# Optimization experiments

Hardware: AMD Instinct MI355X
Metric: run time of the kernel (lower is better)

The kernel has to match this reference:

```python
import jax, jax.numpy as jnp
import numpy as np

DIM = 1024
SCALE = DIM ** (-0.5)
TEMPERATURE = 1.0


def setup_inputs() -> dict:
    key = jax.random.key(0)
    ks = jax.random.split(key, 7)
    B, N, D = 8, 4096, DIM
    s = 1.0 / np.sqrt(D)
    return {
        "x": jax.random.normal(ks[0], (B, N, D), dtype=jnp.float32),
        "Wq": jax.random.normal(ks[1], (D, D), dtype=jnp.float32) * s,
        "bq": jax.random.normal(ks[2], (D,), dtype=jnp.float32) * 0.01,
        "Wk": jax.random.normal(ks[3], (D, D), dtype=jnp.float32) * s,
        "bk": jax.random.normal(ks[4], (D,), dtype=jnp.float32) * 0.01,
        "Wv": jax.random.normal(ks[5], (D, D), dtype=jnp.float32) * s,
        "bv": jax.random.normal(ks[6], (D,), dtype=jnp.float32) * 0.01,
    }


def reference(x, Wq, bq, Wk, bk, Wv, bv):
    B, N, D = x.shape
    # adaptive_avg_pool1d from N -> N//2 with N even == mean over adjacent pairs
    q_input = x.reshape(B, N // 2, 2, D).mean(axis=2)  # [B, N/2, D]
    # torch Linear: y = x @ W.T + b
    q = jnp.einsum("bmd,ed->bme", q_input, Wq) + bq      # [B, N/2, D]
    k = jnp.einsum("bnd,ed->bne", x, Wk) + bk            # [B, N, D]
    v = jnp.einsum("bnd,ed->bne", x, Wv) + bv            # [B, N, D]
    attn = jnp.einsum("bmd,bnd->bmn", q, k) * SCALE      # [B, N/2, N]
    attn = jax.nn.softmax(attn * TEMPERATURE, axis=-1)
    k_out = jnp.einsum("bmn,bnd->bmd", attn, v)          # [B, N/2, D]
    return (q, k_out, k_out)
```

## Files before the change

### kernel.cpp

```cpp
#include <hip/hip_runtime.h>
#include <hip/hip_bf16.h>
#include <cstddef>

typedef __attribute__((ext_vector_type(8))) short s16x8;
typedef __attribute__((ext_vector_type(4))) short s16x4;
typedef __attribute__((ext_vector_type(4))) float f32x4;

#define MFMA_BF16(a, b, c) __builtin_amdgcn_mfma_f32_16x16x32_bf16((a), (b), (c), 0, 0, 0)

__device__ __forceinline__ short f2bf(float f) {
    union { float f; unsigned u; } cv; cv.f = f;
    unsigned u = cv.u;
    unsigned r = (u + 0x7FFFu + ((u >> 16) & 1u)) >> 16;
    return (short)r;
}
__device__ __forceinline__ float bf2f(unsigned short u) {
    union { unsigned u; float f; } cv; cv.u = ((unsigned)u) << 16; return cv.f;
}

__device__ __forceinline__ void gl16(const void* g, void* l) {
    __builtin_amdgcn_global_load_lds(
        (const __attribute__((address_space(1))) void*)g,
        (__attribute__((address_space(3))) void*)l, 16, 0, 0);
}

template <int MODE>
__global__ __launch_bounds__(256, 2) void gemm_bf(
    const void* __restrict__ Ap, const short* __restrict__ Bp,
    const float* __restrict__ bias, const float* __restrict__ lvec,
    void* __restrict__ Cp, void* __restrict__ Cp2,
    int zbase, float* __restrict__ lpart)
{
    constexpr int NT  = (MODE == 4 || MODE == 7) ? 64 : 16;
    constexpr int LDA = (MODE == 4 || MODE == 7) ? 4096 : 1024;
    constexpr int LDB = (MODE == 4 || MODE == 7) ? 4096 : 1024;

    __shared__ short As[128 * 64];
    __shared__ short Bs[128 * 64];
    const int tid = threadIdx.x;

    int bx, by, z;
    if constexpr (MODE == 6) {
        const int swz = (blockIdx.x & 7) * 256 + (blockIdx.x >> 3);
        by = swz % 16; bx = (swz / 16) % 32; z = swz / 512 + zbase;
    } else if constexpr (MODE == 7) {
        const int swz = (blockIdx.x & 7) * 64 + (blockIdx.x >> 3);
        by = swz % 16; bx = (swz / 16) % 8; z = swz / 128 + zbase;
    } else if constexpr (MODE == 0) {
        const int swz = (blockIdx.x & 7) * 256 + (blockIdx.x >> 3);
        bx = swz & 7; by = swz >> 3; z = 0;
    } else if constexpr (MODE == 1) {
        const int swz = (blockIdx.x & 7) * 256 + (blockIdx.x >> 3);
        by = swz % 8; bx = (swz / 8) % 32; z = swz / 256;
    } else if constexpr (MODE == 3 || MODE == 4 || MODE == 5) {
        const int n = blockIdx.x;
        z = n & 7; const int m = n >> 3; by = m % 16; bx = m / 16;
    } else { bx = blockIdx.x; by = blockIdx.y; z = blockIdx.z; }

    const int w = tid >> 6, l = tid & 63, l15 = l & 15, lhi = l >> 4;
    const int wy = w >> 1, wx = w & 1;
    const int X = (l15 & 7) << 3;
    const int lr8 = l >> 3, cb = l & 7, scb = cb ^ lr8;

    size_t arow0 = (size_t)by * 128, brow0 = (size_t)bx * 128;
    if constexpr (MODE == 3 || MODE == 4 || MODE == 5 || MODE == 6) arow0 += (size_t)z * 2048;
    if constexpr (MODE == 7) arow0 += (size_t)(z & 3) * 2048;
    if constexpr (MODE == 1 || MODE == 3 || MODE == 5 || MODE == 6) brow0 += (size_t)z * 4096;
    if constexpr (MODE == 4 || MODE == 7) brow0 += (size_t)z * 1024;

    const short* Ab = (const short*)Ap;
    const float* Af = (const float*)Ap;

    const short* gA = Ab + (arow0 + w * 32 + lr8) * (size_t)LDA + scb * 8;
    const short* gB = Bp + (brow0 + w * 32 + lr8) * (size_t)LDB + scb * 8;

    f32x4 acc[4][4];
    #pragma unroll
    for (int m = 0; m < 4; ++m)
        #pragma unroll
        for (int n = 0; n < 4; ++n) acc[m][n] = (f32x4){0.f, 0.f, 0.f, 0.f};

    const int r0b = tid >> 3, cb8 = (tid & 7) * 8;
    const int r0f = tid >> 4, kcs = tid & 15;

    for (int kt = 0; kt < NT; ++kt) {
        #pragma unroll
        for (int i = 0; i < 4; ++i)
            gl16(gB + (size_t)(i * 8) * LDB + kt * 64, &Bs[(w * 32 + i * 8) * 64]);
        if constexpr (MODE == 2) {
            #pragma unroll
            for (int p = 0; p < 4; ++p) {
                const int r = r0b + p * 32;
                const size_t g = (arow0 + r) * 2048 + kt * 64 + cb8;
                s16x8 u0 = *(const s16x8*)(Ab + g);
                s16x8 u1 = *(const s16x8*)(Ab + g + 1024);
                s16x8 o;
                #pragma unroll
                for (int j = 0; j < 8; ++j)
                    o[j] = f2bf(0.5f * (bf2f((unsigned short)u0[j]) + bf2f((unsigned short)u1[j])));
                *(s16x8*)&As[r * 64 + (cb8 ^ ((r & 7) * 8))] = o;
            }
        } else if constexpr (MODE == 3) {
            const int k0 = kt * 64 + kcs * 4;
            #pragma unroll
            for (int p = 0; p < 8; ++p) {
                const int r = r0f + p * 16;
                float4 u = *(const float4*)(Af + (arow0 + r) * 1024 + k0);
                s16x4 sa = { f2bf(u.x * 0.03125f), f2bf(u.y * 0.03125f),
                             f2bf(u.z * 0.03125f), f2bf(u.w * 0.03125f) };
                *(s16x4*)&As[r * 64 + ((kcs * 4) ^ ((r & 7) * 8))] = sa;
            }
        } else {
            #pragma unroll
            for (int i = 0; i < 4; ++i)
                gl16(gA + (size_t)(i * 8) * LDA + kt * 64, &As[(w * 32 + i * 8) * 64]);
        }
        __syncthreads();
        #pragma unroll
        for (int kk = 0; kk < 2; ++kk) {
            const int e = (kk * 32 + lhi * 8) ^ X;
            s16x8 af[4], bfr[4];
            #pragma unroll
            for (int m = 0; m < 4; ++m)
                af[m] = *(const s16x8*)&As[(wy * 64 + m * 16 + l15) * 64 + e];
            #pragma unroll
            for (int n = 0; n < 4; ++n)
                bfr[n] = *(const s16x8*)&Bs[(wx * 64 + n * 16 + l15) * 64 + e];
            #pragma unroll
            for (int m = 0; m < 4; ++m)
                #pragma unroll
                for (int n = 0; n < 4; ++n)
                    acc[m][n] = MFMA_BF16(af[m], bfr[n], acc[m][n]);
        }
        __syncthreads();
    }

    #pragma unroll
    for (int m = 0; m < 4; ++m) {
        #pragma unroll
        for (int j = 0; j < 4; ++j) {
            const int rl = wy * 64 + m * 16 + lhi * 4 + j;
            const int grow = by * 128 + rl;
            float radd = 0.f, rmul = 1.f;
            if constexpr (MODE == 1) radd = bias[grow];
            if constexpr (MODE == 4 || MODE == 7) rmul = 1.0f / lvec[(size_t)z * 2048 + grow];
            if constexpr (MODE == 6) {
                float s = 0.f;
                #pragma unroll
                for (int n = 0; n < 4; ++n) {
                    const int gcol = bx * 128 + wx * 64 + n * 16 + l15;
                    const float pv = __expf(acc[m][n][j]);
                    s += pv;
                    ((short*)Cp)[(size_t)(z & 3) * 8388608 + (size_t)grow * 4096 + gcol] = f2bf(pv);
                }
                s += __shfl_xor(s, 1);
                s += __shfl_xor(s, 2);
                s += __shfl_xor(s, 4);
                s += __shfl_xor(s, 8);
                if (l15 == 0)
                    lpart[((size_t)(z & 3) * 2048 + grow) * 64 + bx * 2 + wx] = s;
            } else {
                #pragma unroll
                for (int n = 0; n < 4; ++n) {
                    const int cl = wx * 64 + n * 16 + l15;
                    const int gcol = bx * 128 + cl;
                    float v = acc[m][n][j];
                    if constexpr (MODE == 0) {
                        ((short*)Cp)[(size_t)grow * 1024 + gcol] = f2bf(v + bias[gcol]);
                    } else if constexpr (MODE == 1) {
                        ((short*)Cp)[(size_t)z * 4194304 + (size_t)grow * 4096 + gcol] = f2bf(v + radd);
                    } else if constexpr (MODE == 2) {
                        const float qv = v + bias[gcol];
                        ((float*)Cp)[(size_t)grow * 1024 + gcol] = qv;
                        if (Cp2 != nullptr)
                            ((short*)Cp2)[(size_t)grow * 1024 + gcol] = f2bf(qv * 0.03125f);
                    } else if constexpr (MODE == 8) {
                        const float qv = v + bias[gcol];
                        ((float*)Cp)[(size_t)grow * 1024 + gcol] = qv;
                        ((short*)Cp2)[(size_t)grow * 1024 + gcol] = f2bf(qv * 0.03125f);
                    } else if constexpr (MODE == 3 || MODE == 5) {
                        ((short*)Cp)[(size_t)z * 8388608 + (size_t)grow * 4096 + gcol] = f2bf(v);
                    } else {
                        const size_t o = ((size_t)z * 2048 + grow) * 1024 + gcol;
                        const float ov = v * rmul;
                        ((float*)Cp)[o] = ov;
                        ((float*)Cp2)[o] = ov;
                    }
                }
            }
        }
    }
}

__global__ __launch_bounds__(256, 4) void reduce_l(
    const float* __restrict__ lpart, float* __restrict__ lvec, int zbase)
{
    const int r = blockIdx.x * 256 + threadIdx.x;
    const float4* p = (const float4*)(lpart + (size_t)r * 64);
    float s = 0.f;
    #pragma unroll
    for (int i = 0; i < 16; ++i) { float4 v = p[i]; s += v.x + v.y + v.z + v.w; }
    lvec[(size_t)zbase * 2048 + r] = s;
}

template <int MODE>
__global__ __launch_bounds__(256, 2) void gemm_f32(
    const float* __restrict__ Ap, const float* __restrict__ Bp,
    const float* __restrict__ bias, void* __restrict__ Cp, void* __restrict__ Cp2)
{
    constexpr int LDA = (MODE == 2) ? 2048 : 1024;
    __shared__ short As[128 * 64];
    __shared__ short Bs[128 * 64];
    const int tid = threadIdx.x;
    const int bx = blockIdx.x, by = blockIdx.y, z = blockIdx.z;
    const int w = tid >> 6, l = tid & 63, l15 = l & 15, lhi = l >> 4;
    const int wy = w >> 1, wx = w & 1;
    const int X = (l15 & 7) << 3;

    size_t arow0 = (size_t)by * 128, brow0 = (size_t)bx * 128;
    if constexpr (MODE == 1) brow0 += (size_t)z * 4096;

    f32x4 acc[4][4];
    #pragma unroll
    for (int m = 0; m < 4; ++m)
        #pragma unroll
        for (int n = 0; n < 4; ++n) acc[m][n] = (f32x4){0.f, 0.f, 0.f, 0.f};

    const int r0f = tid >> 4, kcs = tid & 15;
    float4 ra[8], ra2[8], rb[8];

    auto load_tile = [&](int kt) {
        const int k0 = kt * 64 + kcs * 4;
        #pragma unroll
        for (int p = 0; p < 8; ++p) {
            const int r = r0f + p * 16;
            if constexpr (MODE == 2) {
                const float* s0 = Ap + (arow0 + r) * (size_t)LDA + k0;
                ra[p] = *(const float4*)s0;
                ra2[p] = *(const float4*)(s0 + 1024);
            } else {
                ra[p] = *(const float4*)(Ap + (arow0 + r) * (size_t)LDA + k0);
            }
            rb[p] = *(const float4*)(Bp + (brow0 + r) * (size_t)1024 + k0);
        }
    };

    load_tile(0);
    for (int kt = 0; kt < 16; ++kt) {
        #pragma unroll
        for (int p = 0; p < 8; ++p) {
            const int r = r0f + p * 16;
            const int e = (kcs * 4) ^ ((r & 7) << 3);
            float ax, ay, az, aw;
            if constexpr (MODE == 2) {
                ax = 0.5f * (ra[p].x + ra2[p].x); ay = 0.5f * (ra[p].y + ra2[p].y);
                az = 0.5f * (ra[p].z + ra2[p].z); aw = 0.5f * (ra[p].w + ra2[p].w);
            } else {
                ax = ra[p].x; ay = ra[p].y; az = ra[p].z; aw = ra[p].w;
            }
            s16x4 sa = { f2bf(ax), f2bf(ay), f2bf(az), f2bf(aw) };
            *(s16x4*)&As[r * 64 + e] = sa;
            s16x4 sb = { f2bf(rb[p].x), f2bf(rb[p].y), f2bf(rb[p].z), f2bf(rb[p].w) };
            *(s16x4*)&Bs[r * 64 + e] = sb;
        }
        if (kt + 1 < 16) load_tile(kt + 1);
        __syncthreads();
        #pragma unroll
        for (int kk = 0; kk < 2; ++kk) {
            const int e = (kk * 32 + lhi * 8) ^ X;
            s16x8 af[4], bfr[4];
            #pragma unroll
            for (int m = 0; m < 4; ++m)
                af[m] = *(const s16x8*)&As[(wy * 64 + m * 16 + l15) * 64 + e];
            #pragma unroll
            for (int n = 0; n < 4; ++n)
                bfr[n] = *(const s16x8*)&Bs[(wx * 64 + n * 16 + l15) * 64 + e];
            #pragma unroll
            for (int m = 0; m < 4; ++m)
                #pragma unroll
                for (int n = 0; n < 4; ++n)
                    acc[m][n] = MFMA_BF16(af[m], bfr[n], acc[m][n]);
        }
        __syncthreads();
    }

    #pragma unroll
    for (int m = 0; m < 4; ++m) {
        #pragma unroll
        for (int j = 0; j < 4; ++j) {
            const int rl = wy * 64 + m * 16 + lhi * 4 + j;
            const int grow = by * 128 + rl;
            const float radd = (MODE == 1) ? bias[grow] : 0.f;
            #pragma unroll
            for (int n = 0; n < 4; ++n) {
                const int cl = wx * 64 + n * 16 + l15;
                const int gcol = bx * 128 + cl;
                float v = acc[m][n][j];
                if constexpr (MODE == 0) {
                    ((short*)Cp)[(size_t)grow * 1024 + gcol] = f2bf(v + bias[gcol]);
                } else if constexpr (MODE == 1) {
                    ((short*)Cp)[(size_t)z * 4194304 + (size_t)grow * 4096 + gcol] = f2bf(v + radd);
                } else {
                    const float q = v + bias[gcol];
                    ((float*)Cp)[(size_t)grow * 1024 + gcol] = q;
                    ((short*)Cp2)[(size_t)grow * 1024 + gcol] = f2bf(q * 0.03125f);
                }
            }
        }
    }
}

__global__ __launch_bounds__(256, 4) void convert_x2(
    const float* __restrict__ x, short* __restrict__ xb, short* __restrict__ xpb)
{
    const int gid = blockIdx.x * 256 + threadIdx.x;
    const int prow = gid >> 7;
    const size_t c8 = (size_t)(gid & 127) * 8;
    const float* p0 = x + (size_t)(2 * prow) * 1024 + c8;
    float4 a0 = *(const float4*)p0, b0 = *(const float4*)(p0 + 4);
    float4 a1 = *(const float4*)(p0 + 1024), b1 = *(const float4*)(p0 + 1028);
    s16x8 o0 = { f2bf(a0.x), f2bf(a0.y), f2bf(a0.z), f2bf(a0.w),
                 f2bf(b0.x), f2bf(b0.y), f2bf(b0.z), f2bf(b0.w) };
    s16x8 o1 = { f2bf(a1.x), f2bf(a1.y), f2bf(a1.z), f2bf(a1.w),
                 f2bf(b1.x), f2bf(b1.y), f2bf(b1.z), f2bf(b1.w) };
    s16x8 op = { f2bf(0.5f * (a0.x + a1.x)), f2bf(0.5f * (a0.y + a1.y)),
                 f2bf(0.5f * (a0.z + a1.z)), f2bf(0.5f * (a0.w + a1.w)),
                 f2bf(0.5f * (b0.x + b1.x)), f2bf(0.5f * (b0.y + b1.y)),
                 f2bf(0.5f * (b0.z + b1.z)), f2bf(0.5f * (b0.w + b1.w)) };
    *(s16x8*)(xb + (size_t)(2 * prow) * 1024 + c8) = o0;
    *(s16x8*)(xb + (size_t)(2 * prow + 1) * 1024 + c8) = o1;
    *(s16x8*)(xpb + (size_t)prow * 1024 + c8) = op;
}

__global__ __launch_bounds__(256, 4) void convert_x(const float* __restrict__ x,
                                                    short* __restrict__ xb)
{
    const size_t i0 = ((size_t)blockIdx.x * 256 + threadIdx.x) * 8;
    float4 a = *(const float4*)(x + i0), b = *(const float4*)(x + i0 + 4);
    s16x8 o = { f2bf(a.x), f2bf(a.y), f2bf(a.z), f2bf(a.w),
                f2bf(b.x), f2bf(b.y), f2bf(b.z), f2bf(b.w) };
    *(s16x8*)(xb + i0) = o;
}

__global__ __launch_bounds__(256, 4) void convert_w(
    const float* __restrict__ Wq, const float* __restrict__ Wk,
    const float* __restrict__ Wv, short* __restrict__ Wb)
{
    const int gid = blockIdx.x * 256 + threadIdx.x;
    const int seg = gid >> 17;
    const size_t off = (size_t)(gid & 131071) * 8;
    const float* s = (seg == 0) ? Wq : ((seg == 1) ? Wk : Wv);
    float4 a = *(const float4*)(s + off), b = *(const float4*)(s + off + 4);
    s16x8 o = { f2bf(a.x), f2bf(a.y), f2bf(a.z), f2bf(a.w),
                f2bf(b.x), f2bf(b.y), f2bf(b.z), f2bf(b.w) };
    *(s16x8*)(Wb + (size_t)seg * 1048576 + off) = o;
}

__global__ __launch_bounds__(256, 4) void softmax_rows(
    const unsigned short* __restrict__ Sin, unsigned short* __restrict__ Pout,
    float* __restrict__ lvec)
{
    const int w = threadIdx.x >> 6, l = threadIdx.x & 63;
    const int row = blockIdx.x * 4 + w;
    const unsigned short* rp = Sin + (size_t)row * 4096;
    unsigned short* wp = Pout + (size_t)row * 4096;

    s16x8 v[8];
    #pragma unroll
    for (int c = 0; c < 8; ++c)
        v[c] = *(const s16x8*)(rp + (c * 64 + l) * 8);

    float mx = -1e30f;
    #pragma unroll
    for (int c = 0; c < 8; ++c)
        #pragma unroll
        for (int j = 0; j < 8; ++j)
            mx = fmaxf(mx, bf2f((unsigned short)v[c][j]));
    #pragma unroll
    for (int d = 1; d < 64; d <<= 1) mx = fmaxf(mx, __shfl_xor(mx, d));

    float sum = 0.f;
    #pragma unroll
    for (int c = 0; c < 8; ++c) {
        #pragma unroll
        for (int j = 0; j < 8; ++j) {
            const float p = __expf(bf2f((unsigned short)v[c][j]) - mx);
            sum += p;
            v[c][j] = f2bf(p);
        }
    }
    #pragma unroll
    for (int d = 1; d < 64; d <<= 1) sum += __shfl_xor(sum, d);

    #pragma unroll
    for (int c = 0; c < 8; ++c)
        *(s16x8*)(wp + (c * 64 + l) * 8) = v[c];
    if (l == 0) lvec[row] = sum;
}

__global__ __launch_bounds__(256, 4) void dup_out(
    const float4* __restrict__ O, float4* __restrict__ o1, float4* __restrict__ o2)
{
    const size_t i0 = (size_t)blockIdx.x * 256 + threadIdx.x;
    #pragma unroll
    for (int p = 0; p < 4; ++p) {
        const size_t i = i0 + (size_t)p * 1048576;
        const float4 t = O[i];
        o1[i] = t;
        o2[i] = t;
    }
}

extern "C" void kernel_launch(void* const* d_in, const int* in_sizes, int n_in,
                              void* d_out, int out_size, void* d_ws, size_t ws_size,
                              hipStream_t stream) {
    const float* x  = (const float*)d_in[0];
    const float* Wq = (const float*)d_in[1];
    const float* bq = (const float*)d_in[2];
    const float* Wk = (const float*)d_in[3];
    const float* bk = (const float*)d_in[4];
    const float* Wv = (const float*)d_in[5];
    const float* bv = (const float*)d_in[6];

    float* out   = (float*)d_out;
    float* q_out = out;
    float* out1  = out + (size_t)16777216;
    float* out2  = out + (size_t)33554432;
    short* Smat  = (short*)out1;

    const unsigned long long NEED_A2 = 241434624ULL;
    const unsigned long long NEED_A1 = 207683584ULL;

    if ((unsigned long long)ws_size >= NEED_A2) {
        short* xb  = (short*)d_ws;
        short* Wb  = xb + (size_t)33554432;
        short* kws = Wb + (size_t)3145728;
        short* vT  = kws + (size_t)33554432;
        short* qs  = vT + (size_t)33554432;
        float* lws = (float*)(qs + (size_t)16777216);
        short* xpb = vT;
        short* Pws   = (short*)d_ws;
        float* lpart = (float*)((char*)d_ws + 67108864);

        convert_x2<<<dim3(8192, 1, 1), 256, 0, stream>>>(x, xb, xpb);
        convert_w<<<dim3(1536, 1, 1), 256, 0, stream>>>(Wq, Wk, Wv, Wb);
        gemm_bf<8><<<dim3(8, 128, 1), 256, 0, stream>>>(xpb, Wb, bq, nullptr, (void*)q_out, (void*)qs, 0, nullptr);
        gemm_bf<0><<<dim3(2048, 1, 1), 256, 0, stream>>>(xb, Wb + 1048576, bk, nullptr, (void*)kws, nullptr, 0, nullptr);
        gemm_bf<1><<<dim3(2048, 1, 1), 256, 0, stream>>>(Wb + 2097152, xb, bv, nullptr, (void*)vT, nullptr, 0, nullptr);
        for (int half = 0; half < 2; ++half) {
            const int zb = half * 4;
            gemm_bf<6><<<dim3(2048, 1, 1), 256, 0, stream>>>(qs, kws, nullptr, nullptr, (void*)Pws, nullptr, zb, lpart);
            reduce_l<<<dim3(32, 1, 1), 256, 0, stream>>>(lpart, lws, zb);
            gemm_bf<7><<<dim3(512, 1, 1), 256, 0, stream>>>(Pws, vT, nullptr, lws, (void*)out1, (void*)out2, zb, nullptr);
        }
    } else if ((unsigned long long)ws_size >= NEED_A1) {
        short* xb  = (short*)d_ws;
        short* Wb  = xb + (size_t)33554432;
        short* kws = Wb + (size_t)3145728;
        short* vT  = kws + (size_t)33554432;
        float* lws = (float*)((char*)d_ws + 207618048ULL);
        unsigned short* Pws = (unsigned short*)d_ws;

        convert_x<<<dim3(16384, 1, 1), 256, 0, stream>>>(x, xb);
        convert_w<<<dim3(1536, 1, 1), 256, 0, stream>>>(Wq, Wk, Wv, Wb);
        gemm_bf<0><<<dim3(2048, 1, 1), 256, 0, stream>>>(xb, Wb + 1048576, bk, nullptr, (void*)kws, nullptr, 0, nullptr);
        gemm_bf<1><<<dim3(2048, 1, 1), 256, 0, stream>>>(Wb + 2097152, xb, bv, nullptr, (void*)vT, nullptr, 0, nullptr);
        gemm_bf<2><<<dim3(8, 128, 1), 256, 0, stream>>>(xb, Wb, bq, nullptr, (void*)q_out, nullptr, 0, nullptr);
        gemm_bf<3><<<dim3(4096, 1, 1), 256, 0, stream>>>(q_out, kws, nullptr, nullptr, (void*)Smat, nullptr, 0, nullptr);
        softmax_rows<<<dim3(4096, 1, 1), 256, 0, stream>>>((const unsigned short*)Smat, Pws, lws);
        gemm_bf<4><<<dim3(1024, 1, 1), 256, 0, stream>>>(Pws, vT, nullptr, lws, (void*)out1, (void*)out2, 0, nullptr);
    } else {
        short* kws = (short*)d_ws;
        short* vT  = kws + (size_t)33554432;
        short* qs  = vT + (size_t)33554432;
        float* lws = (float*)((char*)d_ws + 167772160ULL);
        float* Ows = (float*)d_ws;

        gemm_f32<0><<<dim3(8, 256, 1), 256, 0, stream>>>(x, Wk, bk, (void*)kws, nullptr);
        gemm_f32<1><<<dim3(32, 8, 8), 256, 0, stream>>>(Wv, x, bv, (void*)vT, nullptr);
        gemm_f32<2><<<dim3(8, 128, 1), 256, 0, stream>>>(x, Wq, bq, (void*)q_out, (void*)qs);
        gemm_bf<5><<<dim3(4096, 1, 1), 256, 0, stream>>>(qs, kws, nullptr, nullptr, (void*)Smat, nullptr, 0, nullptr);
        softmax_rows<<<dim3(4096, 1, 1), 256, 0, stream>>>((const unsigned short*)Smat, (unsigned short*)Smat, lws);
        gemm_bf<4><<<dim3(1024, 1, 1), 256, 0, stream>>>(Smat, vT, nullptr, lws, (void*)Ows, (void*)Ows, 0, nullptr);
        dup_out<<<dim3(4096, 1, 1), 256, 0, stream>>>((const float4*)Ows, (float4*)out1, (float4*)out2);
    }
}
```

Baseline: 576.8 us.

## Use 256x256-tile 8-wave pipelined kernel for QK^T exp scores

Replaces the 128x128 gemm_bf<6> launch for the Q·K^T scores with a new 512-thread kernel that computes 256x256 output tiles. Each k-step is split into quarter loads into double-buffered LDS, using explicit vmcnt waits, barriers and s_setprio around the MFMA blocks. The epilogue fuses exp, bf16 store and partial row sums as before. The larger tile raises data reuse per LDS load and overlaps global loads with compute. In exchange it holds 128 accumulator registers per thread and uses about 128KB of LDS, which lowers occupancy, and its hand-tuned wait counts are fragile.

```diff
diff --git a/kernel.cpp b/kernel.cpp
--- a/kernel.cpp
+++ b/kernel.cpp
@@ -22,6 +22,149 @@
     __builtin_amdgcn_global_load_lds(
         (const __attribute__((address_space(1))) void*)g,
         (__attribute__((address_space(3))) void*)l, 16, 0, 0);
+}
+
+__global__ __launch_bounds__(512, 2) void g256s(
+    const short* __restrict__ Ap, const short* __restrict__ Bp,
+    short* __restrict__ Cp, int zbase, float* __restrict__ lpart)
+{
+    constexpr int NT = 16;
+    __shared__ short As[2][2][8192];
+    __shared__ short Bs[2][2][8192];
+
+    const int tid = threadIdx.x;
+    const int n = blockIdx.x;
+    const int swz = (n & 7) * 64 + (n >> 3);
+    const int by = swz % 8, bx = (swz / 8) % 16;
+    const int z = swz / 128 + zbase;
+
+    const int w = tid >> 6, l = tid & 63, l15 = l & 15, lhi = l >> 4;
+    const int wr = (w >> 2) & 1, wc = w & 3;
+    const int X = (l15 & 7) << 3;
+    const int lr8 = l >> 3, cb = l & 7, scb = cb ^ lr8;
+
+    const short* srcA = Ap + ((size_t)z * 2048 + (size_t)by * 256) * 1024;
+    const short* srcB = Bp + ((size_t)z * 4096 + (size_t)bx * 256) * 1024;
+
+    f32x4 acc[8][4];
+    #pragma unroll
+    for (int mm = 0; mm < 8; ++mm)
+        #pragma unroll
+        for (int nn = 0; nn < 4; ++nn) acc[mm][nn] = (f32x4){0.f, 0.f, 0.f, 0.f};
+
+    auto STQ = [&](short* buf, const short* src, int half, int t) {
+        #pragma unroll
+        for (int i = 0; i < 2; ++i)
+            gl16(src + (size_t)(half * 128 + w * 16 + i * 8 + lr8) * 1024 + t * 64 + scb * 8,
+                 &buf[(w * 16 + i * 8) * 64]);
+    };
+
+    s16x8 a[4][2], b[2][2];
+    auto RDA = [&](int s, int mh) {
+        #pragma unroll
+        for (int mm = 0; mm < 4; ++mm)
+            #pragma unroll
+            for (int kk = 0; kk < 2; ++kk)
+                a[mm][kk] = *(const s16x8*)&As[s][mh][(wr * 64 + mm * 16 + l15) * 64 + ((kk * 32 + lhi * 8) ^ X)];
+    };
+    auto RDB = [&](int s, int nh) {
+        #pragma unroll
+        for (int nn = 0; nn < 2; ++nn)
+            #pragma unroll
+            for (int kk = 0; kk < 2; ++kk)
+                b[nn][kk] = *(const s16x8*)&Bs[s][nh][(wc * 32 + nn * 16 + l15) * 64 + ((kk * 32 + lhi * 8) ^ X)];
+    };
+    auto MM = [&](int mo, int no) {
+        #pragma unroll
+        for (int mm = 0; mm < 4; ++mm)
+            #pragma unroll
+            for (int nn = 0; nn < 2; ++nn)
+                #pragma unroll
+                for (int kk = 0; kk < 2; ++kk)
+                    acc[mo + mm][no + nn] = MFMA_BF16(a[mm][kk], b[nn][kk], acc[mo + mm][no + nn]);
+    };
+
+    STQ(&Bs[0][0][0], srcB, 0, 0);
+    STQ(&As[0][1][0], srcA, 1, 0);
+    STQ(&As[0][0][0], srcA, 0, 0);
+    STQ(&Bs[0][1][0], srcB, 1, 0);
+    STQ(&Bs[1][0][0], srcB, 0, 1);
+    STQ(&As[1][1][0], srcA, 1, 1);
+
+    for (int t = 0; t < NT; ++t) {
+        const int s = t & 1, sn = s ^ 1;
+        const bool tail = (t >= NT - 2);
+
+        if (t + 1 < NT) STQ(&As[sn][0][0], srcA, 0, t + 1);
+        if (tail) asm volatile("s_waitcnt vmcnt(0)" ::: "memory");
+        else      asm volatile("s_waitcnt vmcnt(8)" ::: "memory");
+        __builtin_amdgcn_s_barrier();
+        RDA(s, 0); RDB(s, 0);
+        asm volatile("s_waitcnt lgkmcnt(0)" ::: "memory");
+        __builtin_amdgcn_sched_barrier(0);
+        __builtin_amdgcn_s_setprio(1);
+        MM(0, 0);
+        __builtin_amdgcn_s_setprio(0);
+        __builtin_amdgcn_s_barrier();
+
+        if (t + 1 < NT) STQ(&Bs[sn][1][0], srcB, 1, t + 1);
+        RDA(s, 1);
+        asm volatile("s_waitcnt lgkmcnt(0)" ::: "memory");
+        __builtin_amdgcn_sched_barrier(0);
+        __builtin_amdgcn_s_setprio(1);
+        MM(4, 0);
+        __builtin_amdgcn_s_setprio(0);
+        __builtin_amdgcn_s_barrier();
+
+        if (t + 2 < NT) STQ(&Bs[s][0][0], srcB, 0, t + 2);
+        if (tail) asm volatile("s_waitcnt vmcnt(0)" ::: "memory");
+        else      asm volatile("s_waitcnt vmcnt(10)" ::: "memory");
+        __builtin_amdgcn_s_barrier();
+        RDB(s, 1);
+        asm volatile("s_waitcnt lgkmcnt(0)" ::: "memory");
+        __builtin_amdgcn_sched_barrier(0);
+        __builtin_amdgcn_s_setprio(1);
+        MM(4, 2);
+        __builtin_amdgcn_s_setprio(0);
+        __builtin_amdgcn_s_barrier();
+
+        if (t + 2 < NT) STQ(&As[s][1][0], srcA, 1, t + 2);
+        RDA(s, 0);
+        asm volatile("s_waitcnt lgkmcnt(0)" ::: "memory");
+        __builtin_amdgcn_sched_barrier(0);
+        __builtin_amdgcn_s_setprio(1);
+        MM(0, 2);
+        __builtin_amdgcn_s_setprio(0);
+        __builtin_amdgcn_s_barrier();
+    }
+
+    #pragma unroll
+    for (int mh = 0; mh < 2; ++mh) {
+        #pragma unroll
+        for (int mm = 0; mm < 4; ++mm) {
+            #pragma unroll
+            for (int j = 0; j < 4; ++j) {
+                const int gr = by * 256 + mh * 128 + wr * 64 + mm * 16 + lhi * 4 + j;
+                float sum = 0.f;
+                #pragma unroll
+                for (int nh = 0; nh < 2; ++nh) {
+                    #pragma unroll
+                    for (int nn = 0; nn < 2; ++nn) {
+                        const int gc = bx * 256 + nh * 128 + wc * 32 + nn * 16 + l15;
+                        const float pv = __expf(acc[mh * 4 + mm][nh * 2 + nn][j]);
+                        sum += pv;
+                        Cp[(size_t)(z & 3) * 8388608 + (size_t)gr * 4096 + gc] = f2bf(pv);
+                    }
+                }
+                sum += __shfl_xor(sum, 1);
+                sum += __shfl_xor(sum, 2);
+                sum += __shfl_xor(sum, 4);
+                sum += __shfl_xor(sum, 8);
+                if (l15 == 0)
+                    lpart[((size_t)(z & 3) * 2048 + gr) * 64 + bx * 4 + wc] = sum;
+            }
+        }
+    }
 }
 
 template <int MODE>
@@ -449,7 +592,7 @@
         gemm_bf<1><<<dim3(2048, 1, 1), 256, 0, stream>>>(Wb + 2097152, xb, bv, nullptr, (void*)vT, nullptr, 0, nullptr);
         for (int half = 0; half < 2; ++half) {
             const int zb = half * 4;
-            gemm_bf<6><<<dim3(2048, 1, 1), 256, 0, stream>>>(qs, kws, nullptr, nullptr, (void*)Pws, nullptr, zb, lpart);
+            g256s<<<dim3(512, 1, 1), 512, 0, stream>>>(qs, kws, Pws, zb, lpart);
             reduce_l<<<dim3(32, 1, 1), 256, 0, stream>>>(lpart, lws, zb);
             gemm_bf<7><<<dim3(512, 1, 1), 256, 0, stream>>>(Pws, vT, nullptr, lws, (void*)out1, (void*)out2, zb, nullptr);
         }
```

Measured after the change: 633.7 us. 1.1x slower.
